# Kernel tuning notes

Measured on AMD Instinct MI355X. Metric: run time of the kernel, lower is better.

## Reference

```python
import jax, jax.numpy as jnp
import numpy as np

EPS = 1e-6
KH = KW = 3  # square kernel the 5-point plus stencil unpacks into


def setup_inputs() -> dict:
    key = jax.random.key(0)
    k1, k2, k3 = jax.random.split(key, 3)
    bs, ci, co, H, W = 8, 256, 256, 128, 128
    x = jax.random.normal(k1, (bs, ci, H, W), dtype=jnp.float32)
    y = jax.random.normal(k2, (bs, ci), dtype=jnp.float32)
    # packed stencil weights (channels_out, channels_in, stencil_size)
    weights = jax.random.normal(k3, (co, ci, 5), dtype=jnp.float32) * 0.02
    # flat indices into the 3x3 kernel for stencil pts (0,1),(1,0),(1,1),(1,2),(2,1)
    stencil_index = jnp.array([1, 3, 4, 5, 7], dtype=jnp.int32)
    return {"x": x, "y": y, "weights": weights, "stencil_index": stencil_index}


def _modulated_lattice_conv(x, y, weights, stencil_index):
    bs, ci, H, W = x.shape
    co = weights.shape[0]
    # StyleGAN2-style modulation: w2 * (w1 + 1)  -> [bs, co, ci, S]
    w = weights[None, :, :, :] * (y[:, None, :, None] + 1.0)
    # demodulation: rsqrt of sum over (in, stencil) dims
    d = jax.lax.rsqrt(jnp.sum(w * w, axis=(2, 3), keepdims=True) + EPS)
    w = w * d
    # fold batch into output channels for groups=batch trick
    w = w.reshape(bs * co, ci, -1)
    # unpack non-square stencil into zero-padded square kernel (irregular scatter)
    full = jnp.zeros((bs * co, ci, KH * KW), dtype=w.dtype)
    full = full.at[:, :, stencil_index].set(w)
    kern = full.reshape(bs * co, ci, KH, KW)
    # grouped conv: input reshaped to (1, bs*ci, H, W), feature_group_count=bs
    out = jax.lax.conv_general_dilated(
        x.reshape(1, bs * ci, H, W), kern,
        window_strides=(1, 1), padding='SAME',
        feature_group_count=bs,
        dimension_numbers=('NCHW', 'OIHW', 'NCHW'))
    return out.reshape(bs, co, H, W)


def reference(x, y, weights, stencil_index):
    return _modulated_lattice_conv(x, y, weights, stencil_index)
```

## Files before the change

### kernel.cpp

```cpp
#include <hip/hip_runtime.h>


typedef short v8s __attribute__((ext_vector_type(8)));
typedef float v4f __attribute__((ext_vector_type(4)));
typedef int   v4i __attribute__((ext_vector_type(4)));

#define BS 8
#define CI 256
#define CO 256
#define HH 128
#define WW 128

#define WF_CK 10240
#define RSTR_B 5632
#define RSTR_I 1408

#define GLOAD_LDS16(g, l)                                                  \
    __builtin_amdgcn_global_load_lds(                                      \
        (__attribute__((address_space(1))) void*)(g),                      \
        (__attribute__((address_space(3))) void*)(l), 16, 0, 0)

__device__ __forceinline__ unsigned short f2bf(float f) {
    unsigned u = __builtin_bit_cast(unsigned, f);
    u += 0x7FFFu + ((u >> 16) & 1u);
    return (unsigned short)(u >> 16);
}

__global__ __launch_bounds__(256) void wprep2_kernel(const float* __restrict__ y,
                                                     const float* __restrict__ wgt,
                                                     short* __restrict__ wfrag) {
    const int bo = blockIdx.x;
    const int b = bo >> 8, o = bo & 255;
    const int ci = threadIdx.x;
    const float ym = y[b * CI + ci] + 1.0f;
    const float* wp = wgt + (o * CI + ci) * 5;
    float w[5];
    float s2 = 0.f;
    #pragma unroll
    for (int s = 0; s < 5; ++s) { w[s] = wp[s]; s2 += w[s] * w[s]; }
    float ss = ym * ym * s2;
    #pragma unroll
    for (int off = 32; off > 0; off >>= 1) ss += __shfl_down(ss, off);
    __shared__ float red[4];
    if ((threadIdx.x & 63) == 0) red[threadIdx.x >> 6] = ss;
    __syncthreads();
    const float tot = red[0] + red[1] + red[2] + red[3];
    const float scale = ym * rsqrtf(tot + 1e-6f);
    const int ot = o >> 6, mt = (o >> 4) & 3, m = o & 15;
    const int ck = ci >> 5, quad = (ci >> 3) & 3, j = ci & 7;
    size_t base = ((size_t)(b * 4 + ot) * 8 + ck) * WF_CK + quad * 128 + m * 8 + j;
    #pragma unroll
    for (int s = 0; s < 5; ++s)
        wfrag[base + (size_t)(s * 4 + mt) * 512] = (short)f2bf(w[s] * scale);
}

__global__ __launch_bounds__(256) void xprep_kernel(const float* __restrict__ x,
                                                    unsigned int* __restrict__ xt) {
    const int bid = blockIdx.x;
    const int b  = bid >> 10;
    const int ck = (bid >> 7) & 7;
    const int h  = bid & 127;
    const int tid = threadIdx.x;
    __shared__ float tr[128 * 33];
    #pragma unroll
    for (int i = 0; i < 16; ++i) {
        int idx = tid + i * 256;
        int c = idx >> 7, px = idx & 127;
        tr[px * 33 + c] = x[((size_t)(b * CI + ck * 32 + c) * HH + h) * WW + px];
    }
    __syncthreads();
    const int px = tid >> 1, half = tid & 1;
    unsigned pk[8];
    #pragma unroll
    for (int k = 0; k < 8; ++k) {
        float f0 = tr[px * 33 + half * 16 + 2 * k];
        float f1 = tr[px * 33 + half * 16 + 2 * k + 1];
        pk[k] = (unsigned)f2bf(f0) | ((unsigned)f2bf(f1) << 16);
    }
    unsigned int* dst = xt + ((size_t)((b * 8 + ck) * 16384 + h * 128 + px)) * 16
                           + half * 8;
    *(v4i*)dst       = (v4i){(int)pk[0], (int)pk[1], (int)pk[2], (int)pk[3]};
    *(v4i*)(dst + 4) = (v4i){(int)pk[4], (int)pk[5], (int)pk[6], (int)pk[7]};
}

__global__ __launch_bounds__(256, 4) void conv3_kernel(const char* __restrict__ xt,
                                                       const short* __restrict__ wfrag,
                                                       float* __restrict__ out) {
    const int b     = blockIdx.z;
    const int ot    = blockIdx.y;
    const int oBase = ot * 64;
    const int st    = blockIdx.x;
    const int r0    = (st >> 1) * 4;
    const int c0    = (st & 1) * 64;
    const bool left = (c0 == 0);

    const int tid  = threadIdx.x;
    const int wid  = tid >> 6;
    const int lane = tid & 63;
    const int l15  = lane & 15;
    const int quad = lane >> 4;

    __shared__ __align__(16) int xs[6 * RSTR_I];

    v4f acc[4][4];
    #pragma unroll
    for (int a = 0; a < 4; ++a)
        #pragma unroll
        for (int n = 0; n < 4; ++n) acc[a][n] = (v4f){0.f, 0.f, 0.f, 0.f};

    const v4i z4 = (v4i){0, 0, 0, 0};
    if (r0 == 0)
        for (int i = tid; i < 264; i += 256) *(v4i*)&xs[i * 4] = z4;
    if (r0 == HH - 4)
        for (int i = tid; i < 264; i += 256) *(v4i*)&xs[5 * RSTR_I + i * 4] = z4;
    if (left && tid < 24) *(v4i*)&xs[(tid >> 2) * RSTR_I + (tid & 3) * 4] = z4;

    const int row = r0 + wid;
    const short* wfb = wfrag + (size_t)(b * 4 + ot) * 8 * WF_CK;
    const bool rz = (!left) && (l15 == 15);
    const int gstartB = left ? 0 : (c0 - 1) * 64;
    const int lshift  = left ? 64 : 0;

    const int dh[5] = {-1, 0, 0, 0, 1};
    const int dw[5] = { 0,-1, 0, 1, 0};

    for (int ck = 0; ck < 8; ++ck) {
        const char* planep = xt + (((size_t)(b * 8 + ck)) << 20);
        #pragma unroll
        for (int rsel = 0; rsel < 2; ++rsel) {
            int rr = wid + rsel * 4;
            if (rr < 6) {
                bool skip = (r0 == 0 && rr == 0) || (r0 == HH - 4 && rr == 5);
                if (!skip) {
                    int gr = r0 - 1 + rr;
                    const char* gb = planep + (size_t)gr * 8192 + gstartB + lane * 16;
                    char* lb = (char*)xs + rr * RSTR_B + lshift;
                    #pragma unroll
                    for (int t = 0; t < 5; ++t)
                        GLOAD_LDS16(gb + t * 1024, lb + t * 1024);
                }
            }
        }
        __syncthreads();

        const short* wfc = wfb + (size_t)ck * WF_CK;
        #pragma unroll
        for (int s = 0; s < 5; ++s) {
            const int xrow = wid + 1 + dh[s];
            const int xc0  = 1 + dw[s];
            v8s af[4];
            #pragma unroll
            for (int mt = 0; mt < 4; ++mt)
                af[mt] = *(const v8s*)(wfc + (size_t)((s * 4 + mt) * 4 + quad) * 128
                                           + l15 * 8);
            #pragma unroll
            for (int nt = 0; nt < 4; ++nt) {
                v4i bi = *(const v4i*)&xs[xrow * RSTR_I + (nt * 16 + l15 + xc0) * 16
                                          + quad * 4];
                if (s == 3 && nt == 3) { if (rz) bi = z4; }
                v8s bfr = __builtin_bit_cast(v8s, bi);
                #pragma unroll
                for (int mt = 0; mt < 4; ++mt)
                    acc[mt][nt] = __builtin_amdgcn_mfma_f32_16x16x32_bf16(
                        af[mt], bfr, acc[mt][nt], 0, 0, 0);
            }
        }
        __syncthreads();
    }

    #pragma unroll
    for (int mt = 0; mt < 4; ++mt)
        #pragma unroll
        for (int nt = 0; nt < 4; ++nt)
            #pragma unroll
            for (int r = 0; r < 4; ++r) {
                int o = oBase + mt * 16 + quad * 4 + r;
                int c = c0 + nt * 16 + l15;
                out[((size_t)(b * CO + o) * HH + row) * WW + c] = acc[mt][nt][r];
            }
}

__global__ __launch_bounds__(256, 4) void conv_kernel(const float* __restrict__ x,
                                                      const short* __restrict__ wfrag,
                                                      float* __restrict__ out) {
    const int b     = blockIdx.z;
    const int ot    = blockIdx.y;
    const int oBase = ot * 64;
    const int st    = blockIdx.x;
    const int r0    = (st >> 1) * 4;
    const int c0    = (st & 1) * 64;
    const int tid  = threadIdx.x;
    const int wid  = tid >> 6;
    const int lane = tid & 63;
    const int l15  = lane & 15;
    const int quad = lane >> 4;
    #define PXS 20
    __shared__ __align__(16) int xs[6 * 66 * PXS];
    v4f acc[4][4];
    #pragma unroll
    for (int a = 0; a < 4; ++a)
        #pragma unroll
        for (int n = 0; n < 4; ++n) acc[a][n] = (v4f){0.f, 0.f, 0.f, 0.f};
    const int row = r0 + wid;
    const short* wfb = wfrag + (size_t)(b * 4 + ot) * 8 * WF_CK;
    const int dh[5] = {-1, 0, 0, 0, 1};
    const int dw[5] = { 0,-1, 0, 1, 0};
    for (int ck = 0; ck < 8; ++ck) {
        const int ic0 = ck * 32;
        #pragma unroll
        for (int t = 0; t < 6; ++t) {
            int idx = tid + t * 256;
            int cp  = idx & 15;
            int tmp = idx >> 4;
            int cq  = tmp & 15;
            int rr  = tmp >> 4;
            int gr  = r0 - 1 + rr;
            v4f a0 = (v4f){0.f, 0.f, 0.f, 0.f}, a1 = a0;
            if (gr >= 0 && gr < HH) {
                const float* xp = x + ((size_t)(b * CI + ic0 + cp * 2) * HH + gr) * WW
                                    + (c0 + cq * 4);
                a0 = *(const v4f*)xp;
                a1 = *(const v4f*)(xp + HH * WW);
            }
            int base = (rr * 66 + cq * 4 + 1) * PXS + cp;
            #pragma unroll
            for (int k = 0; k < 4; ++k)
                xs[base + k * PXS] =
                    (int)((unsigned)f2bf(a0[k]) | ((unsigned)f2bf(a1[k]) << 16));
        }
        if (tid < 192) {
            int cp   = tid & 15;
            int tmp  = tid >> 4;
            int side = (tmp >= 6) ? 1 : 0;
            int rr   = tmp - 6 * side;
            int gr   = r0 - 1 + rr;
            int gc   = side ? (c0 + 64) : (c0 - 1);
            float v0 = 0.f, v1 = 0.f;
            if (gr >= 0 && gr < HH && gc >= 0 && gc < WW) {
                const float* xp = x + ((size_t)(b * CI + ic0 + cp * 2) * HH + gr) * WW + gc;
                v0 = xp[0];
                v1 = xp[HH * WW];
            }
            int col = side ? 65 : 0;
            xs[(rr * 66 + col) * PXS + cp] =
                (int)((unsigned)f2bf(v0) | ((unsigned)f2bf(v1) << 16));
        }
        __syncthreads();
        const short* wfc = wfb + (size_t)ck * WF_CK;
        #pragma unroll
        for (int s = 0; s < 5; ++s) {
            const int xrow = wid + 1 + dh[s];
            const int xc0  = 1 + dw[s];
            v8s af[4];
            #pragma unroll
            for (int mt = 0; mt < 4; ++mt)
                af[mt] = *(const v8s*)(wfc + (size_t)((s * 4 + mt) * 4 + quad) * 128
                                           + l15 * 8);
            #pragma unroll
            for (int nt = 0; nt < 4; ++nt) {
                int px = xrow * 66 + nt * 16 + l15 + xc0;
                v4i bi = *(const v4i*)&xs[px * PXS + quad * 4];
                v8s bfr = __builtin_bit_cast(v8s, bi);
                #pragma unroll
                for (int mt = 0; mt < 4; ++mt)
                    acc[mt][nt] = __builtin_amdgcn_mfma_f32_16x16x32_bf16(
                        af[mt], bfr, acc[mt][nt], 0, 0, 0);
            }
        }
        __syncthreads();
    }
    #pragma unroll
    for (int mt = 0; mt < 4; ++mt)
        #pragma unroll
        for (int nt = 0; nt < 4; ++nt)
            #pragma unroll
            for (int r = 0; r < 4; ++r) {
                int o = oBase + mt * 16 + quad * 4 + r;
                int c = c0 + nt * 16 + l15;
                out[((size_t)(b * CO + o) * HH + row) * WW + c] = acc[mt][nt][r];
            }
}

__global__ __launch_bounds__(256) void demod_kernel(const float* __restrict__ y,
                                                    const float* __restrict__ wgt,
                                                    float* __restrict__ dbuf) {
    const int bo = blockIdx.x;
    const int b = bo >> 8, o = bo & 255;
    const int i = threadIdx.x;
    const float* wp = wgt + (o * CI + i) * 5;
    const float ym = y[b * CI + i] + 1.0f;
    float s2 = 0.f;
    #pragma unroll
    for (int s = 0; s < 5; ++s) { float w = wp[s]; s2 += w * w; }
    float val = ym * ym * s2;
    #pragma unroll
    for (int off = 32; off > 0; off >>= 1) val += __shfl_down(val, off);
    __shared__ float red[4];
    if ((threadIdx.x & 63) == 0) red[threadIdx.x >> 6] = val;
    __syncthreads();
    if (threadIdx.x == 0) dbuf[bo] = rsqrtf(red[0] + red[1] + red[2] + red[3] + 1e-6f);
}

__global__ __launch_bounds__(256) void conv_kernel_fb(const float* __restrict__ x,
                                                      const float* __restrict__ y,
                                                      const float* __restrict__ wgt,
                                                      const float* __restrict__ dbuf,
                                                      float* __restrict__ out) {
    const int b     = blockIdx.z;
    const int oBase = blockIdx.y * 64;
    const int st    = blockIdx.x;
    const int r0    = (st >> 1) * 4;
    const int c0    = (st & 1) * 64;
    const int tid  = threadIdx.x;
    const int wid  = tid >> 6;
    const int lane = tid & 63;
    const int l15  = lane & 15;
    const int quad = lane >> 4;
    __shared__ int   xs4[16 * 412];
    __shared__ short wlds[5 * 4 * 4 * 16 * 8];
    v4f acc[4][4];
    #pragma unroll
    for (int a = 0; a < 4; ++a)
        #pragma unroll
        for (int n = 0; n < 4; ++n) acc[a][n] = (v4f){0.f, 0.f, 0.f, 0.f};
    const int row = r0 + wid;
    for (int ic0 = 0; ic0 < CI; ic0 += 32) {
        for (int t = 0; t < 25; ++t) {
            int idx = tid + t * 256;
            if (idx < 6336) {
                int cp  = idx / 396;
                int rem = idx - cp * 396;
                int rr  = rem / 66;
                int cc  = rem - rr * 66;
                int gr  = r0 - 1 + rr;
                int gc  = c0 - 1 + cc;
                float v0 = 0.f, v1 = 0.f;
                if (gr >= 0 && gr < HH && gc >= 0 && gc < WW) {
                    const float* xp = x + ((size_t)(b * CI + ic0 + cp * 2) * HH + gr) * WW + gc;
                    v0 = xp[0];
                    v1 = xp[HH * WW];
                }
                xs4[cp * 412 + rr * 68 + cc] =
                    (int)((unsigned)f2bf(v0) | ((unsigned)f2bf(v1) << 16));
            }
        }
        #pragma unroll
        for (int p = 0; p < 8; ++p) {
            int pidx = tid + p * 256;
            int ol = pidx >> 5;
            int il = pidx & 31;
            int o  = oBase + ol;
            int ci = ic0 + il;
            float scale = (y[b * CI + ci] + 1.0f) * dbuf[b * CO + o];
            const float* wp = wgt + (o * CI + ci) * 5;
            int base = (((ol >> 4) * 4 + (il >> 3)) * 16 + (ol & 15)) * 8 + (il & 7);
            #pragma unroll
            for (int s = 0; s < 5; ++s)
                wlds[base + s * (4 * 4 * 16 * 8)] = (short)f2bf(wp[s] * scale);
        }
        __syncthreads();
        const int dh[5] = {-1, 0, 0, 0, 1};
        const int dw[5] = { 0,-1, 0, 1, 0};
        #pragma unroll
        for (int s = 0; s < 5; ++s) {
            int xrow = wid + 1 + dh[s];
            int xcb  = l15 + 1 + dw[s];
            v8s af[4];
            #pragma unroll
            for (int mt = 0; mt < 4; ++mt)
                af[mt] = *(const v8s*)&wlds[(((s * 4 + mt) * 4 + quad) * 16 + l15) * 8];
            #pragma unroll
            for (int nt = 0; nt < 4; ++nt) {
                v4i bi;
                #pragma unroll
                for (int p = 0; p < 4; ++p)
                    bi[p] = xs4[(quad * 4 + p) * 412 + xrow * 68 + nt * 16 + xcb];
                v8s bfr = __builtin_bit_cast(v8s, bi);
                #pragma unroll
                for (int mt = 0; mt < 4; ++mt)
                    acc[mt][nt] = __builtin_amdgcn_mfma_f32_16x16x32_bf16(
                        af[mt], bfr, acc[mt][nt], 0, 0, 0);
            }
        }
        __syncthreads();
    }
    #pragma unroll
    for (int mt = 0; mt < 4; ++mt)
        #pragma unroll
        for (int nt = 0; nt < 4; ++nt)
            #pragma unroll
            for (int r = 0; r < 4; ++r) {
                int o = oBase + mt * 16 + quad * 4 + r;
                int c = c0 + nt * 16 + l15;
                out[((size_t)(b * CO + o) * HH + row) * WW + c] = acc[mt][nt][r];
            }
}

extern "C" void kernel_launch(void* const* d_in, const int* in_sizes, int n_in,
                              void* d_out, int out_size, void* d_ws, size_t ws_size,
                              hipStream_t stream) {
    const float* x   = (const float*)d_in[0];
    const float* y   = (const float*)d_in[1];
    const float* wgt = (const float*)d_in[2];
    float* out = (float*)d_out;

    const size_t WF_BYTES = (size_t)BS * 4 * 8 * WF_CK * sizeof(short);
    const size_t XT_OFF   = WF_BYTES + 8192;
    const size_t XT_BYTES = (size_t)BS * 8 * 16384 * 64;
    const size_t NEED_FULL = XT_OFF + XT_BYTES + 1024;
    const size_t NEED_MID  = WF_BYTES + 8192;

    short* wfrag = (short*)d_ws;

    if (ws_size >= NEED_FULL) {
        unsigned int* xt = (unsigned int*)((char*)d_ws + XT_OFF);
        wprep2_kernel<<<dim3(BS * CO), dim3(256), 0, stream>>>(y, wgt, wfrag);
        xprep_kernel<<<dim3(BS * 8 * HH), dim3(256), 0, stream>>>(x, xt);
        conv3_kernel<<<dim3(64, CO / 64, BS), dim3(256), 0, stream>>>(
            (const char*)xt, wfrag, out);
    } else if (ws_size >= NEED_MID) {
        wprep2_kernel<<<dim3(BS * CO), dim3(256), 0, stream>>>(y, wgt, wfrag);
        conv_kernel<<<dim3(64, CO / 64, BS), dim3(256), 0, stream>>>(x, wfrag, out);
    } else {
        float* dbuf = (float*)d_ws;
        demod_kernel<<<dim3(BS * CO), dim3(256), 0, stream>>>(y, wgt, dbuf);
        conv_kernel_fb<<<dim3(64, CO / 64, BS), dim3(256), 0, stream>>>(x, y, wgt, dbuf, out);
    }
}
```

Before: 313.0 us.

## Double-buffer conv LDS tiles, hoist weight fragments, and merge prep kernels

The conv kernel now double-buffers the activation tile in LDS and issues the global-to-LDS load for the next channel chunk while the current chunk's MFMAs run. All 20 weight fragments for a chunk are loaded up front. Occupancy is lowered to 2 blocks per CU to make room for the extra LDS and registers. The weight-prep and x-transpose kernels are merged into one launch, and the transpose now reads x with 16-byte vector loads into a channel-major LDS tile. The aim is to hide load latency and cut launch overhead, but the lower occupancy and higher register pressure could offset the gain.

```diff
diff --git a/kernel.cpp b/kernel.cpp
--- a/kernel.cpp
+++ b/kernel.cpp
@@ -14,6 +14,8 @@
 #define WF_CK 10240
 #define RSTR_B 5632
 #define RSTR_I 1408
+#define XBUF_I (6 * RSTR_I)
+#define XBUF_B (6 * RSTR_B)
 
 #define GLOAD_LDS16(g, l)                                                  \
     __builtin_amdgcn_global_load_lds(                                      \
@@ -24,6 +26,68 @@
     unsigned u = __builtin_bit_cast(unsigned, f);
     u += 0x7FFFu + ((u >> 16) & 1u);
     return (unsigned short)(u >> 16);
+}
+
+__global__ __launch_bounds__(256) void prep_kernel(const float* __restrict__ x,
+                                                   const float* __restrict__ y,
+                                                   const float* __restrict__ wgt,
+                                                   short* __restrict__ wfrag,
+                                                   unsigned int* __restrict__ xt) {
+    __shared__ float tr[32 * 132];
+    __shared__ float red[4];
+
+    if (blockIdx.x < 2048) {
+        const int bo = blockIdx.x;
+        const int b = bo >> 8, o = bo & 255;
+        const int ci = threadIdx.x;
+        const float ym = y[b * CI + ci] + 1.0f;
+        const float* wp = wgt + (o * CI + ci) * 5;
+        float w[5];
+        float s2 = 0.f;
+        #pragma unroll
+        for (int s = 0; s < 5; ++s) { w[s] = wp[s]; s2 += w[s] * w[s]; }
+        float ss = ym * ym * s2;
+        #pragma unroll
+        for (int off = 32; off > 0; off >>= 1) ss += __shfl_down(ss, off);
+        if ((threadIdx.x & 63) == 0) red[threadIdx.x >> 6] = ss;
+        __syncthreads();
+        const float tot = red[0] + red[1] + red[2] + red[3];
+        const float scale = ym * rsqrtf(tot + 1e-6f);
+        const int ot = o >> 6, mt = (o >> 4) & 3, m = o & 15;
+        const int ck = ci >> 5, quad = (ci >> 3) & 3, j = ci & 7;
+        size_t base = ((size_t)(b * 4 + ot) * 8 + ck) * WF_CK + quad * 128 + m * 8 + j;
+        #pragma unroll
+        for (int s = 0; s < 5; ++s)
+            wfrag[base + (size_t)(s * 4 + mt) * 512] = (short)f2bf(w[s] * scale);
+    } else {
+        const int bid = blockIdx.x - 2048;
+        const int b  = bid >> 10;
+        const int ck = (bid >> 7) & 7;
+        const int h  = bid & 127;
+        const int tid = threadIdx.x;
+        #pragma unroll
+        for (int i = 0; i < 4; ++i) {
+            int q  = tid + i * 256;
+            int c  = q >> 5;
+            int qp = q & 31;
+            v4f v = *(const v4f*)&x[((size_t)(b * CI + ck * 32 + c) * HH + h) * WW
+                                    + qp * 4];
+            *(v4f*)&tr[c * 132 + qp * 4] = v;
+        }
+        __syncthreads();
+        const int px = tid >> 1, half = tid & 1;
+        unsigned pk[8];
+        #pragma unroll
+        for (int k = 0; k < 8; ++k) {
+            float f0 = tr[(half * 16 + 2 * k)     * 132 + px];
+            float f1 = tr[(half * 16 + 2 * k + 1) * 132 + px];
+            pk[k] = (unsigned)f2bf(f0) | ((unsigned)f2bf(f1) << 16);
+        }
+        unsigned int* dst = xt + ((size_t)((b * 8 + ck) * 16384 + h * 128 + px)) * 16
+                               + half * 8;
+        *(v4i*)dst       = (v4i){(int)pk[0], (int)pk[1], (int)pk[2], (int)pk[3]};
+        *(v4i*)(dst + 4) = (v4i){(int)pk[4], (int)pk[5], (int)pk[6], (int)pk[7]};
+    }
 }
 
 __global__ __launch_bounds__(256) void wprep2_kernel(const float* __restrict__ y,
@@ -54,36 +118,7 @@
         wfrag[base + (size_t)(s * 4 + mt) * 512] = (short)f2bf(w[s] * scale);
 }
 
-__global__ __launch_bounds__(256) void xprep_kernel(const float* __restrict__ x,
-                                                    unsigned int* __restrict__ xt) {
-    const int bid = blockIdx.x;
-    const int b  = bid >> 10;
-    const int ck = (bid >> 7) & 7;
-    const int h  = bid & 127;
-    const int tid = threadIdx.x;
-    __shared__ float tr[128 * 33];
-    #pragma unroll
-    for (int i = 0; i < 16; ++i) {
-        int idx = tid + i * 256;
-        int c = idx >> 7, px = idx & 127;
-        tr[px * 33 + c] = x[((size_t)(b * CI + ck * 32 + c) * HH + h) * WW + px];
-    }
-    __syncthreads();
-    const int px = tid >> 1, half = tid & 1;
-    unsigned pk[8];
-    #pragma unroll
-    for (int k = 0; k < 8; ++k) {
-        float f0 = tr[px * 33 + half * 16 + 2 * k];
-        float f1 = tr[px * 33 + half * 16 + 2 * k + 1];
-        pk[k] = (unsigned)f2bf(f0) | ((unsigned)f2bf(f1) << 16);
-    }
-    unsigned int* dst = xt + ((size_t)((b * 8 + ck) * 16384 + h * 128 + px)) * 16
-                           + half * 8;
-    *(v4i*)dst       = (v4i){(int)pk[0], (int)pk[1], (int)pk[2], (int)pk[3]};
-    *(v4i*)(dst + 4) = (v4i){(int)pk[4], (int)pk[5], (int)pk[6], (int)pk[7]};
-}
-
-__global__ __launch_bounds__(256, 4) void conv3_kernel(const char* __restrict__ xt,
+__global__ __launch_bounds__(256, 2) void conv3_kernel(const char* __restrict__ xt,
                                                        const short* __restrict__ wfrag,
                                                        float* __restrict__ out) {
     const int b     = blockIdx.z;
@@ -100,7 +135,7 @@
     const int l15  = lane & 15;
     const int quad = lane >> 4;
 
-    __shared__ __align__(16) int xs[6 * RSTR_I];
+    __shared__ __align__(16) int xs[2 * XBUF_I];
 
     v4f acc[4][4];
     #pragma unroll
@@ -109,11 +144,15 @@
         for (int n = 0; n < 4; ++n) acc[a][n] = (v4f){0.f, 0.f, 0.f, 0.f};
 
     const v4i z4 = (v4i){0, 0, 0, 0};
-    if (r0 == 0)
-        for (int i = tid; i < 264; i += 256) *(v4i*)&xs[i * 4] = z4;
-    if (r0 == HH - 4)
-        for (int i = tid; i < 264; i += 256) *(v4i*)&xs[5 * RSTR_I + i * 4] = z4;
-    if (left && tid < 24) *(v4i*)&xs[(tid >> 2) * RSTR_I + (tid & 3) * 4] = z4;
+    #pragma unroll
+    for (int bb = 0; bb < 2; ++bb) {
+        int* xb = xs + bb * XBUF_I;
+        if (r0 == 0)
+            for (int i = tid; i < 264; i += 256) *(v4i*)&xb[i * 4] = z4;
+        if (r0 == HH - 4)
+            for (int i = tid; i < 264; i += 256) *(v4i*)&xb[5 * RSTR_I + i * 4] = z4;
+        if (left && tid < 24) *(v4i*)&xb[(tid >> 2) * RSTR_I + (tid & 3) * 4] = z4;
+    }
 
     const int row = r0 + wid;
     const short* wfb = wfrag + (size_t)(b * 4 + ot) * 8 * WF_CK;
@@ -121,11 +160,9 @@
     const int gstartB = left ? 0 : (c0 - 1) * 64;
     const int lshift  = left ? 64 : 0;
 
-    const int dh[5] = {-1, 0, 0, 0, 1};
-    const int dw[5] = { 0,-1, 0, 1, 0};
-
-    for (int ck = 0; ck < 8; ++ck) {
-        const char* planep = xt + (((size_t)(b * 8 + ck)) << 20);
+    auto stage = [&](int ckk, int bufsel) {
+        const char* planep = xt + (((size_t)(b * 8 + ckk)) << 20);
+        char* lbase = (char*)xs + bufsel * XBUF_B;
         #pragma unroll
         for (int rsel = 0; rsel < 2; ++rsel) {
             int rr = wid + rsel * 4;
@@ -134,35 +171,48 @@
                 if (!skip) {
                     int gr = r0 - 1 + rr;
                     const char* gb = planep + (size_t)gr * 8192 + gstartB + lane * 16;
-                    char* lb = (char*)xs + rr * RSTR_B + lshift;
+                    char* lb = lbase + rr * RSTR_B + lshift;
                     #pragma unroll
                     for (int t = 0; t < 5; ++t)
                         GLOAD_LDS16(gb + t * 1024, lb + t * 1024);
                 }
             }
         }
-        __syncthreads();
-
+    };
+
+    stage(0, 0);
+    __syncthreads();
+
+    const int dh[5] = {-1, 0, 0, 0, 1};
+    const int dw[5] = { 0,-1, 0, 1, 0};
+
+    #pragma unroll 2
+    for (int ck = 0; ck < 8; ++ck) {
         const short* wfc = wfb + (size_t)ck * WF_CK;
+        const int* xb = xs + (ck & 1) * XBUF_I;
+
+        v8s af[20];
+        #pragma unroll
+        for (int sm = 0; sm < 20; ++sm)
+            af[sm] = *(const v8s*)(wfc + (size_t)(sm * 4 + quad) * 128 + l15 * 8);
+        __builtin_amdgcn_sched_barrier(0);
+
+        if (ck < 7) stage(ck + 1, (ck + 1) & 1);
+
         #pragma unroll
         for (int s = 0; s < 5; ++s) {
             const int xrow = wid + 1 + dh[s];
             const int xc0  = 1 + dw[s];
-            v8s af[4];
-            #pragma unroll
-            for (int mt = 0; mt < 4; ++mt)
-                af[mt] = *(const v8s*)(wfc + (size_t)((s * 4 + mt) * 4 + quad) * 128
-                                           + l15 * 8);
             #pragma unroll
             for (int nt = 0; nt < 4; ++nt) {
-                v4i bi = *(const v4i*)&xs[xrow * RSTR_I + (nt * 16 + l15 + xc0) * 16
+                v4i bi = *(const v4i*)&xb[xrow * RSTR_I + (nt * 16 + l15 + xc0) * 16
                                           + quad * 4];
                 if (s == 3 && nt == 3) { if (rz) bi = z4; }
                 v8s bfr = __builtin_bit_cast(v8s, bi);
                 #pragma unroll
                 for (int mt = 0; mt < 4; ++mt)
                     acc[mt][nt] = __builtin_amdgcn_mfma_f32_16x16x32_bf16(
-                        af[mt], bfr, acc[mt][nt], 0, 0, 0);
+                        af[s * 4 + mt], bfr, acc[mt][nt], 0, 0, 0);
             }
         }
         __syncthreads();
@@ -414,8 +464,8 @@
 
     if (ws_size >= NEED_FULL) {
         unsigned int* xt = (unsigned int*)((char*)d_ws + XT_OFF);
-        wprep2_kernel<<<dim3(BS * CO), dim3(256), 0, stream>>>(y, wgt, wfrag);
-        xprep_kernel<<<dim3(BS * 8 * HH), dim3(256), 0, stream>>>(x, xt);
+        prep_kernel<<<dim3(2048 + BS * 8 * HH), dim3(256), 0, stream>>>(
+            x, y, wgt, wfrag, xt);
         conv3_kernel<<<dim3(64, CO / 64, BS), dim3(256), 0, stream>>>(
             (const char*)xt, wfrag, out);
     } else if (ws_size >= NEED_MID) {
```

After: 312.3 us. About the same (-0.2%).
